# Performance work log

Hardware: AMD Instinct MI355X
Metric: run time of the kernel (lower is better)

Reference implementation:

```python
import jax, jax.numpy as jnp
import numpy as np

SIM_THRES = 0.9
CLASS_SPEC = True
CIN, COUT, K, H, W_DIM = 256, 64, 1024, 200, 400


def setup_inputs() -> dict:
    key = jax.random.key(0)
    k1, k2, k3, k4, k5 = jax.random.split(key, 5)
    idx_feat = jax.random.normal(k1, (1, CIN, K, 1), jnp.float32)
    x = jax.random.normal(k2, (1, COUT, H * W_DIM), jnp.float32)
    W = jax.random.normal(k3, (COUT, CIN), jnp.float32) * 0.01  # conv1x1 weight, init std=0.01
    b = jnp.zeros((COUT,), jnp.float32)
    pred_cate = jax.random.randint(k4, (K,), 0, 80)
    pred_score = jax.random.uniform(k5, (K,), jnp.float32)
    return {"x": x, "idx_feat": idx_feat, "pred_cate": pred_cate,
            "pred_score": pred_score, "W": W, "b": b, "n": 1, "h": H, "w": W_DIM}


def reference(x, idx_feat, pred_cate, pred_score, W, b, n, h, w):
    # 1x1 conv -> reshape -> permute: meta_weight [K, Cout]
    feat = idx_feat[0, :, :, 0]                      # [Cin, K]
    mw = feat.T @ W.T + b                            # [K, Cout]
    # cosine similarity (row-normalized, clamp min 1e-8)
    nrm = jnp.linalg.norm(mw, axis=1, keepdims=True)
    a = mw / jnp.maximum(nrm, 1e-8)
    sim = a @ a.T                                    # [K, K]
    label = jnp.triu(sim >= SIM_THRES)
    if CLASS_SPEC:
        label = label & (pred_cate[:, None] == pred_cate[None, :])
    # cumsum-based greedy Matrix-NMS-style dedup
    cum = jnp.cumsum(label.astype(jnp.float32), axis=0) < 2.0
    keep = jnp.diagonal(cum)                         # [K] bool keep mask
    # masked rows instead of boolean indexing (jit-static shapes);
    # non-kept rows are zeroed and their norm replaced by 1 to avoid 0/0.
    lm = (label & cum).astype(jnp.float32) * keep[:, None].astype(jnp.float32)
    ln = lm.sum(axis=1, keepdims=True)
    merged = (lm @ mw) / jnp.where(ln > 0, ln, 1.0)  # [K, Cout]
    inst = jnp.einsum('kc,ncp->nkp', merged, x).reshape(n, -1, h, w)
    return inst, keep, pred_cate, pred_score
```

## Files before the change

### kernel.cpp

```cpp
#include <hip/hip_runtime.h>
#include <math.h>

#define CIN 256
#define COUT 64
#define KN 1024
#define PN 80000
#define SIMT 0.9f

__global__ __launch_bounds__(256) void k_mw(const float* __restrict__ idx_feat,
                                            const float* __restrict__ W,
                                            const float* __restrict__ b,
                                            float* __restrict__ mw,
                                            float* __restrict__ a) {
    int t = threadIdx.x;
    int id = blockIdx.x * 256 + t;
    int k = id >> 6;
    int o = id & 63;
    const float4* W4 = (const float4*)W;
    float acc = 0.f;
    #pragma unroll 4
    for (int c4 = 0; c4 < 64; ++c4) {
        float4 wv = W4[o * 64 + c4];
        int c = c4 * 4;
        acc += idx_feat[(c + 0) * KN + k] * wv.x
             + idx_feat[(c + 1) * KN + k] * wv.y
             + idx_feat[(c + 2) * KN + k] * wv.z
             + idx_feat[(c + 3) * KN + k] * wv.w;
    }
    float v = acc + b[o];
    mw[k * COUT + o] = v;
    float ss = v * v;
    #pragma unroll
    for (int m = 1; m < 64; m <<= 1) ss += __shfl_xor(ss, m, 64);
    float nrm = sqrtf(ss);
    a[k * COUT + o] = v / fmaxf(nrm, 1e-8f);
}

__global__ __launch_bounds__(256) void k_label(const float* __restrict__ a,
                                               const int* __restrict__ cate,
                                               unsigned int* __restrict__ mask,
                                               unsigned int* __restrict__ keep) {
    int j = blockIdx.x;
    int t = threadIdx.x;
    __shared__ __align__(16) float ajs[64];
    __shared__ int cnts[256];
    __shared__ unsigned int mws[32];
    if (t < 64) ajs[t] = a[j * 64 + t];
    if (t < 32) mws[t] = 0u;
    __syncthreads();
    int cj = cate[j];
    const float4* a4  = (const float4*)a;
    const float4* aj4 = (const float4*)ajs;
    bool lab[4];
    int cnt = 0;
    #pragma unroll
    for (int q = 0; q < 4; ++q) {
        int i = t * 4 + q;
        float s = 0.f;
        #pragma unroll
        for (int c4 = 0; c4 < 16; ++c4) {
            float4 av = a4[i * 16 + c4];
            float4 jv = aj4[c4];
            s += av.x * jv.x + av.y * jv.y + av.z * jv.z + av.w * jv.w;
        }
        lab[q] = (i <= j) && (s >= SIMT) && (cate[i] == cj);
        cnt += lab[q] ? 1 : 0;
    }
    cnts[t] = cnt;
    __syncthreads();
    for (int off = 1; off < 256; off <<= 1) {
        int v = cnts[t];
        int add = (t >= off) ? cnts[t - off] : 0;
        __syncthreads();
        cnts[t] = v + add;
        __syncthreads();
    }
    int run = cnts[t] - cnt;
    #pragma unroll
    for (int q = 0; q < 4; ++q) {
        int i = t * 4 + q;
        run += lab[q] ? 1 : 0;
        bool cumf = run < 2;
        if (lab[q] && cumf) atomicOr(&mws[i >> 5], 1u << (i & 31));
        if (i == j) keep[j] = cumf ? 1u : 0u;
    }
    __syncthreads();
    if (t < 32) mask[j * 32 + t] = mws[t];
}

__global__ __launch_bounds__(256) void k_merge(const float* __restrict__ mw,
                                               const unsigned int* __restrict__ mask,
                                               const unsigned int* __restrict__ keep,
                                               float* __restrict__ mergedT) {
    int i = blockIdx.x;
    int t = threadIdx.x;
    int c = t & 63, g = t >> 6;
    int wi = i >> 5;
    unsigned int bi = 1u << (i & 31);
    float acc = 0.f;
    int cnt = 0;
    for (int jj = 0; jj < 256; ++jj) {
        int j = g * 256 + jj;
        unsigned int wv = mask[j * 32 + wi];
        if (wv & bi) { acc += mw[j * 64 + c]; cnt++; }
    }
    __shared__ float sa[4][64];
    __shared__ int sc[4];
    sa[g][c] = acc;
    if (c == 0) sc[g] = cnt;
    __syncthreads();
    if (g == 0) {
        float tot = sa[0][c] + sa[1][c] + sa[2][c] + sa[3][c];
        int ct = sc[0] + sc[1] + sc[2] + sc[3];
        float mv = keep[i] ? tot / (float)max(ct, 1) : 0.f;
        mergedT[c * KN + i] = mv;
    }
}

__global__ __launch_bounds__(256) void k_inst(const float* __restrict__ x,
                                              const float* __restrict__ mergedT,
                                              float* __restrict__ out) {
    __shared__ __align__(16) float xt[64 * 256];
    int t = threadIdx.x;
    int pbase = blockIdx.x * 256;
    int kchunk = blockIdx.y;
    #pragma unroll
    for (int it = 0; it < 16; ++it) {
        int idx = it * 256 + t;
        int c = idx >> 6;
        int p4 = (idx & 63) << 2;
        float4 v = make_float4(0.f, 0.f, 0.f, 0.f);
        int p = pbase + p4;
        if (p < PN) v = *(const float4*)(x + c * PN + p);
        *(float4*)(xt + c * 256 + p4) = v;
    }
    __syncthreads();
    int pq = t & 63;
    int kg = t >> 6;
    int p = pbase + pq * 4;
    bool valid = p < PN;
    for (int sub = 0; sub < 4; ++sub) {
        int k0 = kchunk * 256 + sub * 64 + kg * 16;
        float4 acc[16];
        #pragma unroll
        for (int kk = 0; kk < 16; ++kk) acc[kk] = make_float4(0.f, 0.f, 0.f, 0.f);
        #pragma unroll 4
        for (int c = 0; c < 64; ++c) {
            float4 xv = *(const float4*)(xt + c * 256 + pq * 4);
            const float* mrow = mergedT + c * KN + k0;
            #pragma unroll
            for (int kk = 0; kk < 16; ++kk) {
                float m = mrow[kk];
                acc[kk].x += m * xv.x;
                acc[kk].y += m * xv.y;
                acc[kk].z += m * xv.z;
                acc[kk].w += m * xv.w;
            }
        }
        if (valid) {
            #pragma unroll
            for (int kk = 0; kk < 16; ++kk) {
                *(float4*)(out + (long)(k0 + kk) * PN + p) = acc[kk];
            }
        }
    }
}

__global__ void k_tail(const int* __restrict__ cate,
                       const float* __restrict__ score,
                       const unsigned int* __restrict__ keep,
                       float* __restrict__ out) {
    int t = blockIdx.x * 256 + threadIdx.x;
    if (t < KN) {
        long base = (long)KN * PN;
        out[base + t]            = keep[t] ? 1.f : 0.f;
        out[base + KN + t]       = (float)cate[t];
        out[base + 2 * KN + t]   = score[t];
    }
}

extern "C" void kernel_launch(void* const* d_in, const int* in_sizes, int n_in,
                              void* d_out, int out_size, void* d_ws, size_t ws_size,
                              hipStream_t stream) {
    const float* x        = (const float*)d_in[0];
    const float* idx_feat = (const float*)d_in[1];
    const int*   cate     = (const int*)d_in[2];
    const float* score    = (const float*)d_in[3];
    const float* W        = (const float*)d_in[4];
    const float* b        = (const float*)d_in[5];
    float* out = (float*)d_out;

    char* ws = (char*)d_ws;
    float* mw            = (float*)(ws + 0);
    float* a             = (float*)(ws + 262144);
    float* mergedT       = (float*)(ws + 524288);
    unsigned int* mask   = (unsigned int*)(ws + 786432);
    unsigned int* keep   = (unsigned int*)(ws + 917504);

    k_mw   <<<256,  256, 0, stream>>>(idx_feat, W, b, mw, a);
    k_label<<<KN,   256, 0, stream>>>(a, cate, mask, keep);
    k_merge<<<KN,   256, 0, stream>>>(mw, mask, keep, mergedT);
    dim3 gD((PN + 255) / 256, 4);
    k_inst <<<gD,   256, 0, stream>>>(x, mergedT, out);
    k_tail <<<4,    256, 0, stream>>>(cate, score, keep, out);
}
```

Measured before the change: 584.4 us.

## Compute instance projection with bf16 MFMA instead of fp32 FMA

```diff
diff --git a/kernel.cpp b/kernel.cpp
--- a/kernel.cpp
+++ b/kernel.cpp
@@ -6,6 +6,15 @@
 #define KN 1024
 #define PN 80000
 #define SIMT 0.9f
+
+typedef __attribute__((ext_vector_type(8))) short  short8;
+typedef __attribute__((ext_vector_type(4))) float  f32x4;
+
+__device__ inline unsigned short f2bf(float f) {
+    unsigned u = __float_as_uint(f);
+    unsigned r = u + 0x7FFFu + ((u >> 16) & 1u);
+    return (unsigned short)(r >> 16);
+}
 
 __global__ __launch_bounds__(256) void k_mw(const float* __restrict__ idx_feat,
                                             const float* __restrict__ W,
@@ -91,7 +100,7 @@
 __global__ __launch_bounds__(256) void k_merge(const float* __restrict__ mw,
                                                const unsigned int* __restrict__ mask,
                                                const unsigned int* __restrict__ keep,
-                                               float* __restrict__ mergedT) {
+                                               unsigned short* __restrict__ mergedB) {
     int i = blockIdx.x;
     int t = threadIdx.x;
     int c = t & 63, g = t >> 6;
@@ -113,55 +122,45 @@
         float tot = sa[0][c] + sa[1][c] + sa[2][c] + sa[3][c];
         int ct = sc[0] + sc[1] + sc[2] + sc[3];
         float mv = keep[i] ? tot / (float)max(ct, 1) : 0.f;
-        mergedT[c * KN + i] = mv;
+        mergedB[i * 64 + c] = f2bf(mv);
     }
 }
 
 __global__ __launch_bounds__(256) void k_inst(const float* __restrict__ x,
-                                              const float* __restrict__ mergedT,
+                                              const unsigned short* __restrict__ mergedB,
                                               float* __restrict__ out) {
-    __shared__ __align__(16) float xt[64 * 256];
-    int t = threadIdx.x;
-    int pbase = blockIdx.x * 256;
-    int kchunk = blockIdx.y;
-    #pragma unroll
-    for (int it = 0; it < 16; ++it) {
-        int idx = it * 256 + t;
-        int c = idx >> 6;
-        int p4 = (idx & 63) << 2;
-        float4 v = make_float4(0.f, 0.f, 0.f, 0.f);
-        int p = pbase + p4;
-        if (p < PN) v = *(const float4*)(x + c * PN + p);
-        *(float4*)(xt + c * 256 + p4) = v;
-    }
-    __syncthreads();
-    int pq = t & 63;
-    int kg = t >> 6;
-    int p = pbase + pq * 4;
-    bool valid = p < PN;
-    for (int sub = 0; sub < 4; ++sub) {
-        int k0 = kchunk * 256 + sub * 64 + kg * 16;
-        float4 acc[16];
+    int t = threadIdx.x;
+    int lane = t & 63;
+    int wv = t >> 6;
+    int n0 = blockIdx.x * 64 + wv * 16;
+    int m0 = blockIdx.y * 512;
+    int nn = n0 + (lane & 15);
+    int quad = lane >> 4;
+
+    short8 bfr[2];
+    #pragma unroll
+    for (int f = 0; f < 2; ++f) {
         #pragma unroll
-        for (int kk = 0; kk < 16; ++kk) acc[kk] = make_float4(0.f, 0.f, 0.f, 0.f);
-        #pragma unroll 4
-        for (int c = 0; c < 64; ++c) {
-            float4 xv = *(const float4*)(xt + c * 256 + pq * 4);
-            const float* mrow = mergedT + c * KN + k0;
-            #pragma unroll
-            for (int kk = 0; kk < 16; ++kk) {
-                float m = mrow[kk];
-                acc[kk].x += m * xv.x;
-                acc[kk].y += m * xv.y;
-                acc[kk].z += m * xv.z;
-                acc[kk].w += m * xv.w;
-            }
+        for (int j = 0; j < 8; ++j) {
+            int k = f * 32 + quad * 8 + j;
+            bfr[f][j] = (short)f2bf(x[k * PN + nn]);
         }
-        if (valid) {
-            #pragma unroll
-            for (int kk = 0; kk < 16; ++kk) {
-                *(float4*)(out + (long)(k0 + kk) * PN + p) = acc[kk];
-            }
+    }
+
+    int arow_off = quad * 8;
+    #pragma unroll 4
+    for (int mt = 0; mt < 32; ++mt) {
+        int mrow = m0 + mt * 16 + (lane & 15);
+        const unsigned short* ap = mergedB + mrow * 64 + arow_off;
+        short8 a0 = *(const short8*)(ap);
+        short8 a1 = *(const short8*)(ap + 32);
+        f32x4 acc = {0.f, 0.f, 0.f, 0.f};
+        acc = __builtin_amdgcn_mfma_f32_16x16x32_bf16(a0, bfr[0], acc, 0, 0, 0);
+        acc = __builtin_amdgcn_mfma_f32_16x16x32_bf16(a1, bfr[1], acc, 0, 0, 0);
+        int rbase = m0 + mt * 16 + quad * 4;
+        #pragma unroll
+        for (int r = 0; r < 4; ++r) {
+            out[(rbase + r) * PN + nn] = acc[r];
         }
     }
 }
@@ -191,16 +190,16 @@
     float* out = (float*)d_out;
 
     char* ws = (char*)d_ws;
-    float* mw            = (float*)(ws + 0);
-    float* a             = (float*)(ws + 262144);
-    float* mergedT       = (float*)(ws + 524288);
-    unsigned int* mask   = (unsigned int*)(ws + 786432);
-    unsigned int* keep   = (unsigned int*)(ws + 917504);
+    float*          mw      = (float*)(ws + 0);
+    float*          a       = (float*)(ws + 262144);
+    unsigned short* mergedB = (unsigned short*)(ws + 524288);
+    unsigned int*   mask    = (unsigned int*)(ws + 655360);
+    unsigned int*   keep    = (unsigned int*)(ws + 786432);
 
     k_mw   <<<256,  256, 0, stream>>>(idx_feat, W, b, mw, a);
     k_label<<<KN,   256, 0, stream>>>(a, cate, mask, keep);
-    k_merge<<<KN,   256, 0, stream>>>(mw, mask, keep, mergedT);
-    dim3 gD((PN + 255) / 256, 4);
-    k_inst <<<gD,   256, 0, stream>>>(x, mergedT, out);
+    k_merge<<<KN,   256, 0, stream>>>(mw, mask, keep, mergedB);
+    dim3 gD(PN / 64, 2);
+    k_inst <<<gD,   256, 0, stream>>>(x, mergedB, out);
     k_tail <<<4,    256, 0, stream>>>(cate, score, keep, out);
 }
```

Result: faster. 526.4 us (-9.9%).
